# Kernel optimization log

Hardware: AMD Instinct MI355X
Metric: run time of the kernel (lower is better)

The kernel has to match this reference:

```python
import jax, jax.numpy as jnp
import numpy as np

B, S, D_MODEL, N_HEADS, D_FF = 4, 2048, 1024, 16, 4096
HEAD_DIM = D_MODEL // N_HEADS
NUM_BUCKETS, MAX_DISTANCE = 32, 128
EPS = 1e-6


def _relative_position_bucket(relative_position, num_buckets=NUM_BUCKETS, max_distance=MAX_DISTANCE):
    # bidirectional (encoder) variant, matching T5RelativePositionBias
    n = -relative_position
    nb = num_buckets // 2
    ret = (n < 0).astype(jnp.int32) * nb
    n = jnp.abs(n)
    max_exact = nb // 2
    val_if_large = max_exact + (
        jnp.log(jnp.maximum(n, 1).astype(jnp.float32) / max_exact)
        / np.log(max_distance / max_exact) * (nb - max_exact)
    ).astype(jnp.int32)
    val_if_large = jnp.minimum(val_if_large, nb - 1)
    return ret + jnp.where(n < max_exact, n, val_if_large)


def t5_position_bias(rel_emb, q_len, k_len):
    ctx = jnp.arange(q_len)[:, None]
    mem = jnp.arange(k_len)[None, :]
    rp_bucket = _relative_position_bucket(mem - ctx)          # [S, S]
    bias = rel_emb[rp_bucket]                                  # [S, S, H]
    return jnp.transpose(bias, (2, 0, 1))[None]                # [1, H, S, S]


def layer_norm(x, g, b):
    mu = jnp.mean(x, axis=-1, keepdims=True)
    var = jnp.mean(jnp.square(x - mu), axis=-1, keepdims=True)
    return (x - mu) * jax.lax.rsqrt(var + EPS) * g + b


def setup_inputs() -> dict:
    key = jax.random.key(0)
    ks = jax.random.split(key, 20)
    s = 0.02
    p = {
        'src': jax.random.normal(ks[0], (B, S, D_MODEL), jnp.float32),
        'wq': jax.random.normal(ks[1], (D_MODEL, D_MODEL), jnp.float32) * s,
        'bq': jnp.zeros((D_MODEL,), jnp.float32),
        'wk': jax.random.normal(ks[2], (D_MODEL, D_MODEL), jnp.float32) * s,
        'bk': jnp.zeros((D_MODEL,), jnp.float32),
        'wv': jax.random.normal(ks[3], (D_MODEL, D_MODEL), jnp.float32) * s,
        'bv': jnp.zeros((D_MODEL,), jnp.float32),
        'wo': jax.random.normal(ks[4], (D_MODEL, D_MODEL), jnp.float32) * s,
        'bo': jnp.zeros((D_MODEL,), jnp.float32),
        'w1': jax.random.normal(ks[5], (D_MODEL, D_FF), jnp.float32) * s,
        'b1': jnp.zeros((D_FF,), jnp.float32),
        'w2': jax.random.normal(ks[6], (D_FF, D_MODEL), jnp.float32) * s,
        'b2': jnp.zeros((D_MODEL,), jnp.float32),
        'ln1_g': jnp.ones((D_MODEL,), jnp.float32),
        'ln1_b': jnp.zeros((D_MODEL,), jnp.float32),
        'ln2_g': jnp.ones((D_MODEL,), jnp.float32),
        'ln2_b': jnp.zeros((D_MODEL,), jnp.float32),
        'rel_emb': jax.random.normal(ks[7], (NUM_BUCKETS, N_HEADS), jnp.float32) * s,
    }
    return p


def reference(src, wq, bq, wk, bk, wv, bv, wo, bo, w1, b1, w2, b2,
              ln1_g, ln1_b, ln2_g, ln2_b, rel_emb):
    b, s, _ = src.shape

    # --- self-attention block (pre-norm) ---
    xn = layer_norm(src, ln1_g, ln1_b)
    q = (xn @ wq + bq).reshape(b, s, N_HEADS, HEAD_DIM).transpose(0, 2, 1, 3)
    k = (xn @ wk + bk).reshape(b, s, N_HEADS, HEAD_DIM).transpose(0, 2, 1, 3)
    v = (xn @ wv + bv).reshape(b, s, N_HEADS, HEAD_DIM).transpose(0, 2, 1, 3)

    bias = t5_position_bias(rel_emb, s, s)                       # [1,H,S,S]
    scores = jnp.einsum('bhqd,bhkd->bhqk', q, k) / np.sqrt(HEAD_DIM) + bias
    attn = jax.nn.softmax(scores, axis=-1)
    ctx = jnp.einsum('bhqk,bhkd->bhqd', attn, v)                 # [B,H,S,Dh]
    ctx = ctx.transpose(0, 2, 1, 3).reshape(b, s, D_MODEL)
    x = src + (ctx @ wo + bo)

    # --- FFN block (pre-norm, ReLU) ---
    yn = layer_norm(x, ln2_g, ln2_b)
    y = jax.nn.relu(yn @ w1 + b1) @ w2 + b2
    return x + y
```

## Files before the change

### kernel.cpp

```cpp
#include <hip/hip_runtime.h>
#include <math.h>

typedef unsigned short u16;

#define S_LEN 2048
#define BSZ 4
#define DM 1024
#define NH 16
#define HD 64
#define DFF 4096
#define ROWS (BSZ * S_LEN)
#define LOG2E 1.4426950408889634f

typedef __attribute__((__ext_vector_type__(8))) __bf16 bf16x8;
typedef __attribute__((__ext_vector_type__(8))) short short8;
typedef __attribute__((__ext_vector_type__(4))) short short4v;
typedef __attribute__((__ext_vector_type__(4))) float f32x4;
typedef __attribute__((__ext_vector_type__(4))) float float4v;

__device__ __forceinline__ float bf2f(u16 u) {
    union { unsigned int i; float f; } c; c.i = ((unsigned int)u) << 16; return c.f;
}
__device__ __forceinline__ u16 f2bf(float f) {
    union { float f; unsigned int i; } c; c.f = f;
    unsigned int r = c.i + 0x7fffu + ((c.i >> 16) & 1u);
    return (u16)(r >> 16);
}
__device__ __forceinline__ u16 f2bf_rn(float f) {
    union { float f; unsigned int i; } c; c.f = f;
    return (u16)((c.i + 0x8000u) >> 16);
}
__device__ __forceinline__ float ldin(const void* p, long i, int f32) {
    return f32 ? ((const float*)p)[i] : bf2f(((const u16*)p)[i]);
}
__device__ __forceinline__ int dtype_f32(const u16* ln1g) {
    return ln1g[0] != 0x3F80;
}
__device__ __forceinline__ void gl_lds16(const void* g, void* l) {
    __builtin_amdgcn_global_load_lds(
        (const __attribute__((address_space(1))) unsigned int*)g,
        (__attribute__((address_space(3))) unsigned int*)l, 16, 0, 0);
}

#define DPP_ADD(x, ctrl) { int _v = __builtin_bit_cast(int, x);                         \
    float _y = __builtin_bit_cast(float, __builtin_amdgcn_mov_dpp(_v, ctrl, 0xF, 0xF, true)); \
    x = x + _y; }

__device__ __forceinline__ void tr_tile(
    const void* __restrict__ src, u16* __restrict__ dst, int N, int K,
    int bx, int by, int f32, int tid, u16 (*t)[72])
{
#pragma unroll
    for (int i = 0; i < 2; i++) {
        int c = tid + i * 256;
        int row = c >> 3, col = (c & 7) * 8;
        long off = (long)(by * 64 + row) * N + bx * 64 + col;
        short8 v;
        if (f32) {
            const float* s = (const float*)src + off;
            float4v a = *(const float4v*)s;
            float4v b = *(const float4v*)(s + 4);
#pragma unroll
            for (int k = 0; k < 4; k++) { v[k] = (short)f2bf(a[k]); v[k + 4] = (short)f2bf(b[k]); }
        } else {
            v = *(const short8*)((const u16*)src + off);
        }
        *(short8*)(&t[row][col]) = v;
    }
    __syncthreads();
#pragma unroll
    for (int i = 0; i < 2; i++) {
        int c = tid + i * 256;
        int row = c >> 3, col = (c & 7) * 8;
        short8 v;
#pragma unroll
        for (int jj = 0; jj < 8; jj++) v[jj] = (short)t[col + jj][row];
        *(short8*)(dst + (long)(bx * 64 + row) * K + by * 64 + col) = v;
    }
}

__global__ __launch_bounds__(256) void transpose4(
    const void* wq, const void* wk, const void* wv, const void* wo,
    u16* __restrict__ wqkvt, u16* __restrict__ wot, const u16* __restrict__ ln1g)
{
    __shared__ u16 t[64][72];
    int z = blockIdx.z;
    const void* src = (z == 0) ? wq : (z == 1) ? wk : (z == 2) ? wv : wo;
    u16* dst = (z < 3) ? wqkvt + (long)z * 1024 * 1024 : wot;
    tr_tile(src, dst, DM, DM, blockIdx.x, blockIdx.y, dtype_f32(ln1g), threadIdx.x, t);
}

__global__ __launch_bounds__(256) void transpose2(
    const void* w1, const void* w2, u16* __restrict__ w1t, u16* __restrict__ w2t,
    const u16* __restrict__ ln1g)
{
    __shared__ u16 t[64][72];
    int f32 = dtype_f32(ln1g);
    if (blockIdx.z == 0)
        tr_tile(w1, w1t, DFF, DM, blockIdx.x, blockIdx.y, f32, threadIdx.x, t);
    else
        tr_tile(w2, w2t, DM, DFF, blockIdx.y, blockIdx.x, f32, threadIdx.x, t);
}

__global__ __launch_bounds__(256) void vtrans(
    const u16* __restrict__ v, u16* __restrict__ vt)
{
    __shared__ u16 t[64][72];
    int s0 = blockIdx.x * 64;
    int bh = blockIdx.y;
    const u16* src = v + (long)bh * S_LEN * HD;
    u16* dst = vt + (long)bh * HD * S_LEN;
    int tid = threadIdx.x;
#pragma unroll
    for (int i = 0; i < 2; i++) {
        int c = tid + i * 256;
        int row = c >> 3, col = (c & 7) * 8;
        *(short8*)(&t[row][col]) = *(const short8*)(src + (long)(s0 + row) * HD + col);
    }
    __syncthreads();
#pragma unroll
    for (int i = 0; i < 2; i++) {
        int c = tid + i * 256;
        int row = c >> 3, col = (c & 7) * 8;
        short8 o;
#pragma unroll
        for (int jj = 0; jj < 8; jj++) o[jj] = (short)t[col + jj][row];
        *(short8*)(dst + (long)row * S_LEN + s0 + col) = o;
    }
}

__global__ __launch_bounds__(256) void prep_kernel(
    const void* bq, const void* bk, const void* bv, const void* bo,
    const void* b1, const void* b2, const void* l1g, const void* l1b,
    const void* l2g, const void* l2b, const void* rel,
    u16* __restrict__ smalls, float* __restrict__ bias_full)
{
    int f32 = dtype_f32((const u16*)l1g);
    int tid = blockIdx.x * blockDim.x + threadIdx.x;
    if (tid < 13312) {
        float v;
        if      (tid < 1024)  v = ldin(bq,  tid,         f32);
        else if (tid < 2048)  v = ldin(bk,  tid - 1024,  f32);
        else if (tid < 3072)  v = ldin(bv,  tid - 2048,  f32);
        else if (tid < 4096)  v = ldin(bo,  tid - 3072,  f32);
        else if (tid < 8192)  v = ldin(b1,  tid - 4096,  f32);
        else if (tid < 9216)  v = ldin(b2,  tid - 8192,  f32);
        else if (tid < 10240) v = ldin(l1g, tid - 9216,  f32);
        else if (tid < 11264) v = ldin(l1b, tid - 10240, f32);
        else if (tid < 12288) v = ldin(l2g, tid - 11264, f32);
        else                  v = ldin(l2b, tid - 12288, f32);
        smalls[tid] = f2bf(v);
    }
    if (tid < 4095 * 16) {
        int dIdx = tid >> 4;
        int h = tid & 15;
        int delta = dIdx - 2047;
        int n = -delta;
        int ret = (n < 0) ? 16 : 0;
        int na = (n < 0) ? -n : n;
        int bkt;
        if (na < 8) {
            bkt = na;
        } else {
            float tval = logf((float)na * 0.125f) * 2.8853900817779268f;
            int v = 8 + (int)tval;
            bkt = v < 15 ? v : 15;
        }
        bkt += ret;
        bias_full[h * 4095 + dIdx] = ldin(rel, bkt * 16 + h, f32) * LOG2E;
    }
}

__global__ __launch_bounds__(256) void ln_kernel(
    const void* __restrict__ xin, int external, const u16* __restrict__ ln1g,
    const u16* __restrict__ g, const u16* __restrict__ bta, u16* __restrict__ out)
{
    int f32 = external ? dtype_f32(ln1g) : 0;
    int row = blockIdx.x;
    int tid = threadIdx.x;
    float vals[4];
    if (f32) {
        float4v v = *(const float4v*)((const float*)xin + (long)row * DM + tid * 4);
#pragma unroll
        for (int k = 0; k < 4; k++) vals[k] = v[k];
    } else {
        short4v v = *(const short4v*)((const u16*)xin + (long)row * DM + tid * 4);
#pragma unroll
        for (int k = 0; k < 4; k++) vals[k] = bf2f((u16)v[k]);
    }
    float s1 = 0.f, s2 = 0.f;
#pragma unroll
    for (int k = 0; k < 4; k++) { s1 += vals[k]; s2 += vals[k] * vals[k]; }
#pragma unroll
    for (int off = 32; off > 0; off >>= 1) {
        s1 += __shfl_xor(s1, off);
        s2 += __shfl_xor(s2, off);
    }
    __shared__ float ps1[4], ps2[4];
    int wave = tid >> 6, lane = tid & 63;
    if (lane == 0) { ps1[wave] = s1; ps2[wave] = s2; }
    __syncthreads();
    s1 = ps1[0] + ps1[1] + ps1[2] + ps1[3];
    s2 = ps2[0] + ps2[1] + ps2[2] + ps2[3];
    float mu = s1 * (1.0f / DM);
    float var = s2 * (1.0f / DM) - mu * mu;
    float rs = rsqrtf(var + 1e-6f);
    short4v ov;
#pragma unroll
    for (int k = 0; k < 4; k++) {
        float gv = bf2f(g[tid * 4 + k]);
        float bv = bf2f(bta[tid * 4 + k]);
        ov[k] = (short)f2bf((vals[k] - mu) * rs * gv + bv);
    }
    *(short4v*)(out + (long)row * DM + tid * 4) = ov;
}

#define BM 128
#define BN 128
#define BK 64

__global__ __launch_bounds__(256, 3) void gemm_bt(
    const u16* __restrict__ A, const u16* __restrict__ Bt,
    const u16* __restrict__ bias, int M, int N, int K, int mode,
    u16* __restrict__ out_q, u16* __restrict__ out_k, u16* __restrict__ out_v,
    const void* __restrict__ res, void* __restrict__ outp,
    const u16* __restrict__ ln1g)
{
    __shared__ u16 As[BM][BK];
    __shared__ u16 Bs[BN][BK];
    int tid = threadIdx.x;
    int wave = tid >> 6, lane = tid & 63;
    int quad = lane >> 4, l16 = lane & 15;
    int wr = (wave >> 1) * 64, wc = (wave & 1) * 64;
    long m0 = (long)blockIdx.y * BM, n0 = (long)blockIdx.x * BN;
    int flg = (mode == 2 || mode == 4) ? dtype_f32(ln1g) : 0;

    int prow = tid >> 3;
    int pchk = tid & 7;
    int cchk = pchk ^ (prow & 7);
    int skc = cchk * 8;
    int pkc = pchk * 8;
    int rxor = l16 & 7;

    f32x4 acc[4][4];
    f32x4 z = {0.f, 0.f, 0.f, 0.f};
#pragma unroll
    for (int i = 0; i < 4; i++)
#pragma unroll
        for (int j = 0; j < 4; j++) acc[i][j] = z;

    for (int k0 = 0; k0 < K; k0 += BK) {
        __syncthreads();
#pragma unroll
        for (int ro = 0; ro < 4; ro++) {
            gl_lds16(A  + (m0 + ro * 32 + prow) * K + k0 + skc, &As[ro * 32 + prow][pkc]);
            gl_lds16(Bt + (n0 + ro * 32 + prow) * K + k0 + skc, &Bs[ro * 32 + prow][pkc]);
        }
        __syncthreads();
#pragma unroll
        for (int t = 0; t < 2; t++) {
            int rc = ((t * 4 + quad) ^ rxor) * 8;
            bf16x8 af[4], bfr[4];
#pragma unroll
            for (int i = 0; i < 4; i++)
                af[i] = __builtin_bit_cast(bf16x8, *(const short8*)(&As[wr + i * 16 + l16][rc]));
#pragma unroll
            for (int j = 0; j < 4; j++)
                bfr[j] = __builtin_bit_cast(bf16x8, *(const short8*)(&Bs[wc + j * 16 + l16][rc]));
#pragma unroll
            for (int i = 0; i < 4; i++)
#pragma unroll
                for (int j = 0; j < 4; j++)
                    acc[i][j] = __builtin_amdgcn_mfma_f32_16x16x32_bf16(af[i], bfr[j], acc[i][j], 0, 0, 0);
        }
    }

#pragma unroll
    for (int i = 0; i < 4; i++) {
#pragma unroll
        for (int j = 0; j < 4; j++) {
#pragma unroll
            for (int r = 0; r < 4; r++) {
                long gr = m0 + wr + i * 16 + quad * 4 + r;
                long gc = n0 + wc + j * 16 + l16;
                float val = acc[i][j][r] + bf2f(bias[gc]);
                if (mode == 1) {
                    int sel = (int)(gc >> 10);
                    int cc = (int)(gc & 1023);
                    int h = cc >> 6, d = cc & 63;
                    int b = (int)(gr >> 11), s = (int)(gr & 2047);
                    u16* dst = (sel == 0) ? out_q : (sel == 1 ? out_k : out_v);
                    dst[(((long)(b * NH + h)) * S_LEN + s) * HD + d] = f2bf(val);
                } else if (mode == 2) {
                    long idx = gr * N + gc;
                    float rv = flg ? ((const float*)res)[idx]
                                   : bf2f(((const u16*)res)[idx]);
                    ((u16*)outp)[idx] = f2bf(val + rv);
                } else if (mode == 3) {
                    ((u16*)outp)[gr * N + gc] = f2bf(val > 0.f ? val : 0.f);
                } else {
                    long idx = gr * N + gc;
                    float o = val + bf2f(((const u16*)res)[idx]);
                    if (flg) ((float*)outp)[idx] = o;
                    else     ((u16*)outp)[idx]  = f2bf(o);
                }
            }
        }
    }
}

__global__ __launch_bounds__(256, 4) void attn_kernel(
    const u16* __restrict__ Qg, const u16* __restrict__ Kg, const u16* __restrict__ Vtg,
    const float* __restrict__ bias_full, u16* __restrict__ ctx)
{
    __shared__ u16 Ks[64][64];
    __shared__ u16 Vt[64][64];
    __shared__ u16 Ps[64][72];
    __shared__ float bias_l[2112];
    __shared__ float l_sh[64];

    int bh = blockIdx.y;
    int b = bh >> 4, h = bh & 15;
    int q0 = blockIdx.x * 64;
    const u16* Q  = Qg  + (long)bh * S_LEN * HD;
    const u16* Kp = Kg  + (long)bh * S_LEN * HD;
    const u16* Vp = Vtg + (long)bh * HD * S_LEN;

    int tid = threadIdx.x;
    int wave = tid >> 6, lane = tid & 63;
    int quad = lane >> 4, l16 = lane & 15;

    for (int i = tid; i < 2112; i += 256)
        bias_l[i] = bias_full[h * 4095 + 1984 + i - q0];
    float Bneg = bias_full[h * 4095 + 0];
    float Bpos = bias_full[h * 4095 + 4094];

    int prow = tid >> 3, pchk = tid & 7;
    int cchk = pchk ^ (prow & 7);
    int rxor = l16 & 7;
    int rc0 = (quad ^ rxor) * 8;
    int rc1 = ((4 + quad) ^ rxor) * 8;

    bf16x8 aq[2];
#pragma unroll
    for (int t = 0; t < 2; t++)
        aq[t] = __builtin_bit_cast(bf16x8,
            *(const short8*)(Q + (long)(q0 + wave * 16 + l16) * HD + t * 32 + quad * 8));

    f32x4 o[4];
    f32x4 z = {0.f, 0.f, 0.f, 0.f};
#pragma unroll
    for (int j = 0; j < 4; j++) o[j] = z;
    float l_acc = 0.f;

    int ib = 63 + quad * 4 - wave * 16 - l16;
    const float c0 = 0.125f * LOG2E;

    for (int t0 = 0; t0 < S_LEN; t0 += 64) {
        __syncthreads();
#pragma unroll
        for (int ro = 0; ro < 2; ro++) {
            gl_lds16(Kp + (long)(t0 + ro * 32 + prow) * HD + cchk * 8,
                     &Ks[ro * 32 + prow][pchk * 8]);
            gl_lds16(Vp + (long)(ro * 32 + prow) * S_LEN + t0 + cchk * 8,
                     &Vt[ro * 32 + prow][pchk * 8]);
        }
        __syncthreads();

        f32x4 s_[4];
#pragma unroll
        for (int j = 0; j < 4; j++) {
            f32x4 a = z;
            bf16x8 kf0 = __builtin_bit_cast(bf16x8, *(const short8*)(&Ks[j * 16 + l16][rc0]));
            a = __builtin_amdgcn_mfma_f32_16x16x32_bf16(kf0, aq[0], a, 0, 0, 0);
            bf16x8 kf1 = __builtin_bit_cast(bf16x8, *(const short8*)(&Ks[j * 16 + l16][rc1]));
            a = __builtin_amdgcn_mfma_f32_16x16x32_bf16(kf1, aq[1], a, 0, 0, 0);
            s_[j] = a;
        }
        int d0 = t0 - q0;
        int nearb = (d0 >= -153 && d0 <= 153);
        float bconst = (d0 > 0) ? Bpos : Bneg;
#pragma unroll
        for (int j = 0; j < 4; j++) {
            short4v pk;
#pragma unroll
            for (int r = 0; r < 4; r++) {
                float bl = nearb ? bias_l[ib + t0 + j * 16 + r] : bconst;
                float p = exp2f(fminf(fmaf(s_[j][r], c0, bl), 100.0f));
                l_acc += p;
                pk[r] = (short)f2bf_rn(p);
            }
            *(short4v*)(&Ps[wave * 16 + l16][j * 16 + quad * 4]) = pk;
        }

        bf16x8 ap[2];
#pragma unroll
        for (int tt = 0; tt < 2; tt++)
            ap[tt] = __builtin_bit_cast(bf16x8,
                *(const short8*)(&Ps[wave * 16 + l16][tt * 32 + quad * 8]));
#pragma unroll
        for (int j = 0; j < 4; j++) {
            f32x4 t = o[j];
            bf16x8 bv0 = __builtin_bit_cast(bf16x8, *(const short8*)(&Vt[j * 16 + l16][rc0]));
            t = __builtin_amdgcn_mfma_f32_16x16x32_bf16(ap[0], bv0, t, 0, 0, 0);
            bf16x8 bv1 = __builtin_bit_cast(bf16x8, *(const short8*)(&Vt[j * 16 + l16][rc1]));
            t = __builtin_amdgcn_mfma_f32_16x16x32_bf16(ap[1], bv1, t, 0, 0, 0);
            o[j] = t;
        }
    }

    l_acc += __shfl_xor(l_acc, 16);
    l_acc += __shfl_xor(l_acc, 32);
    l_sh[wave * 16 + l16] = l_acc;
#pragma unroll
    for (int r = 0; r < 4; r++) {
        int qr = wave * 16 + quad * 4 + r;
        float linv = 1.0f / l_sh[qr];
        long srow = (long)(b * S_LEN + q0 + qr);
#pragma unroll
        for (int j = 0; j < 4; j++)
            ctx[srow * DM + h * HD + j * 16 + l16] = f2bf(o[j][r] * linv);
    }
}

extern "C" void kernel_launch(void* const* d_in, const int* in_sizes, int n_in,
                              void* d_out, int out_size, void* d_ws, size_t ws_size,
                              hipStream_t stream)
{
    const void* src  = d_in[0];
    const void* wq   = d_in[1];
    const void* bq   = d_in[2];
    const void* wk   = d_in[3];
    const void* bk   = d_in[4];
    const void* wv   = d_in[5];
    const void* bv   = d_in[6];
    const void* wo   = d_in[7];
    const void* bo   = d_in[8];
    const void* w1   = d_in[9];
    const void* b1   = d_in[10];
    const void* w2   = d_in[11];
    const void* b2   = d_in[12];
    const void* ln1g = d_in[13];
    const void* ln1b = d_in[14];
    const void* ln2g = d_in[15];
    const void* ln2b = d_in[16];
    const void* rel  = d_in[17];
    const u16* l1g16 = (const u16*)ln1g;

    char* ws = (char*)d_ws;
    const long MB = 1L << 20;
    u16*   smalls = (u16*)  (ws);
    float* bfull  = (float*)(ws + 65536);
    u16*   xn     = (u16*)  (ws + 1  * MB);
    u16*   vtg    = (u16*)  (ws + 1  * MB);
    u16*   qws    = (u16*)  (ws + 17 * MB);
    u16*   kws    = (u16*)  (ws + 33 * MB);
    u16*   vws    = (u16*)  (ws + 49 * MB);
    u16*   hbuf   = (u16*)  (ws + 1  * MB);
    u16*   ctx    = (u16*)  (ws + 65 * MB);
    u16*   yn     = (u16*)  (ws + 65 * MB);
    u16*   xbf    = (u16*)  (ws + 81 * MB);
    u16*   wqkvt  = (u16*)  (ws + 97 * MB);
    u16*   wot    = (u16*)  (ws + 103 * MB);
    u16*   w1t    = (u16*)  (ws + 97 * MB);
    u16*   w2t    = (u16*)  (ws + 105 * MB);

    transpose4<<<dim3(16, 16, 4), 256, 0, stream>>>(wq, wk, wv, wo, wqkvt, wot, l1g16);
    prep_kernel<<<256, 256, 0, stream>>>(bq, bk, bv, bo, b1, b2,
                                         ln1g, ln1b, ln2g, ln2b, rel,
                                         smalls, bfull);

    ln_kernel<<<ROWS, 256, 0, stream>>>(src, 1, l1g16,
                                        smalls + 9216, smalls + 10240, xn);

    gemm_bt<<<dim3(3072 / BN, ROWS / BM), 256, 0, stream>>>(
        xn, wqkvt, smalls + 0, ROWS, 3072, DM, 1,
        qws, kws, vws, nullptr, nullptr, l1g16);

    vtrans<<<dim3(S_LEN / 64, BSZ * NH), 256, 0, stream>>>(vws, vtg);

    attn_kernel<<<dim3(S_LEN / 64, BSZ * NH), 256, 0, stream>>>(qws, kws, vtg, bfull, ctx);

    gemm_bt<<<dim3(DM / BN, ROWS / BM), 256, 0, stream>>>(
        ctx, wot, smalls + 3072, ROWS, DM, DM, 2,
        nullptr, nullptr, nullptr, src, xbf, l1g16);

    transpose2<<<dim3(64, 16, 2), 256, 0, stream>>>(w1, w2, w1t, w2t, l1g16);

    ln_kernel<<<ROWS, 256, 0, stream>>>(xbf, 0, l1g16,
                                        smalls + 11264, smalls + 12288, yn);

    gemm_bt<<<dim3(DFF / BN, ROWS / BM), 256, 0, stream>>>(
        yn, w1t, smalls + 4096, ROWS, DFF, DM, 3,
        nullptr, nullptr, nullptr, nullptr, hbuf, l1g16);

    gemm_bt<<<dim3(DM / BN, ROWS / BM), 256, 0, stream>>>(
        hbuf, w2t, smalls + 8192, ROWS, DM, DFF, 4,
        nullptr, nullptr, nullptr, xbf, d_out, l1g16);
}
```

Baseline: 628.5 us.

## Compute softmax row sums via MFMA, store bias as bf16, swizzle GEMM blocks

The attention kernel now computes the softmax denominator with an extra MFMA against a ones vector, removing the scalar accumulation and the cross-lane shuffle/LDS reduction. It also uses the hardware exp2 intrinsic and a native bf16 conversion, and stores the position bias in LDS as bf16 to shrink the shared-memory footprint. Separately, the GEMM remaps block IDs in an XCD-style swizzle to improve L2 locality. The changes trade a little bias precision and two extra MFMAs per tile for fewer VALU ops and less LDS.

Measured after the change: 597.4 us. 1.05x faster.

```diff
diff --git a/kernel.cpp b/kernel.cpp
--- a/kernel.cpp
+++ b/kernel.cpp
@@ -26,9 +26,9 @@
     unsigned int r = c.i + 0x7fffu + ((c.i >> 16) & 1u);
     return (u16)(r >> 16);
 }
-__device__ __forceinline__ u16 f2bf_rn(float f) {
-    union { float f; unsigned int i; } c; c.f = f;
-    return (u16)((c.i + 0x8000u) >> 16);
+__device__ __forceinline__ u16 f2bf_cvt(float f) {
+    __bf16 h = (__bf16)f;
+    return __builtin_bit_cast(u16, h);
 }
 __device__ __forceinline__ float ldin(const void* p, long i, int f32) {
     return f32 ? ((const float*)p)[i] : bf2f(((const u16*)p)[i]);
@@ -41,10 +41,6 @@
         (const __attribute__((address_space(1))) unsigned int*)g,
         (__attribute__((address_space(3))) unsigned int*)l, 16, 0, 0);
 }
-
-#define DPP_ADD(x, ctrl) { int _v = __builtin_bit_cast(int, x);                         \
-    float _y = __builtin_bit_cast(float, __builtin_amdgcn_mov_dpp(_v, ctrl, 0xF, 0xF, true)); \
-    x = x + _y; }
 
 __device__ __forceinline__ void tr_tile(
     const void* __restrict__ src, u16* __restrict__ dst, int N, int K,
@@ -232,7 +228,14 @@
     int wave = tid >> 6, lane = tid & 63;
     int quad = lane >> 4, l16 = lane & 15;
     int wr = (wave >> 1) * 64, wc = (wave & 1) * 64;
-    long m0 = (long)blockIdx.y * BM, n0 = (long)blockIdx.x * BN;
+
+    int nwg = gridDim.x * gridDim.y;
+    int bid = blockIdx.y * gridDim.x + blockIdx.x;
+    int chunk = nwg >> 3;
+    int swz = (bid & 7) * chunk + (bid >> 3);
+    int bx = swz % gridDim.x, by = swz / gridDim.x;
+
+    long m0 = (long)by * BM, n0 = (long)bx * BN;
     int flg = (mode == 2 || mode == 4) ? dtype_f32(ln1g) : 0;
 
     int prow = tid >> 3;
@@ -316,8 +319,7 @@
     __shared__ u16 Ks[64][64];
     __shared__ u16 Vt[64][64];
     __shared__ u16 Ps[64][72];
-    __shared__ float bias_l[2112];
-    __shared__ float l_sh[64];
+    __shared__ u16 bias_s[2112];
 
     int bh = blockIdx.y;
     int b = bh >> 4, h = bh & 15;
@@ -331,7 +333,7 @@
     int quad = lane >> 4, l16 = lane & 15;
 
     for (int i = tid; i < 2112; i += 256)
-        bias_l[i] = bias_full[h * 4095 + 1984 + i - q0];
+        bias_s[i] = f2bf(bias_full[h * 4095 + 1984 + i - q0]);
     float Bneg = bias_full[h * 4095 + 0];
     float Bpos = bias_full[h * 4095 + 4094];
 
@@ -347,11 +349,15 @@
         aq[t] = __builtin_bit_cast(bf16x8,
             *(const short8*)(Q + (long)(q0 + wave * 16 + l16) * HD + t * 32 + quad * 8));
 
+    bf16x8 ones;
+#pragma unroll
+    for (int i = 0; i < 8; i++) ones[i] = (__bf16)1.0f;
+
     f32x4 o[4];
     f32x4 z = {0.f, 0.f, 0.f, 0.f};
 #pragma unroll
     for (int j = 0; j < 4; j++) o[j] = z;
-    float l_acc = 0.f;
+    f32x4 lacc = z;
 
     int ib = 63 + quad * 4 - wave * 16 - l16;
     const float c0 = 0.125f * LOG2E;
@@ -385,10 +391,9 @@
             short4v pk;
 #pragma unroll
             for (int r = 0; r < 4; r++) {
-                float bl = nearb ? bias_l[ib + t0 + j * 16 + r] : bconst;
-                float p = exp2f(fminf(fmaf(s_[j][r], c0, bl), 100.0f));
-                l_acc += p;
-                pk[r] = (short)f2bf_rn(p);
+                float bl = nearb ? bf2f(bias_s[ib + t0 + j * 16 + r]) : bconst;
+                float p = __builtin_amdgcn_exp2f(fminf(fmaf(s_[j][r], c0, bl), 100.0f));
+                pk[r] = (short)f2bf_cvt(p);
             }
             *(short4v*)(&Ps[wave * 16 + l16][j * 16 + quad * 4]) = pk;
         }
@@ -398,6 +403,8 @@
         for (int tt = 0; tt < 2; tt++)
             ap[tt] = __builtin_bit_cast(bf16x8,
                 *(const short8*)(&Ps[wave * 16 + l16][tt * 32 + quad * 8]));
+        lacc = __builtin_amdgcn_mfma_f32_16x16x32_bf16(ap[0], ones, lacc, 0, 0, 0);
+        lacc = __builtin_amdgcn_mfma_f32_16x16x32_bf16(ap[1], ones, lacc, 0, 0, 0);
 #pragma unroll
         for (int j = 0; j < 4; j++) {
             f32x4 t = o[j];
@@ -409,13 +416,10 @@
         }
     }
 
-    l_acc += __shfl_xor(l_acc, 16);
-    l_acc += __shfl_xor(l_acc, 32);
-    l_sh[wave * 16 + l16] = l_acc;
 #pragma unroll
     for (int r = 0; r < 4; r++) {
         int qr = wave * 16 + quad * 4 + r;
-        float linv = 1.0f / l_sh[qr];
+        float linv = 1.0f / lacc[r];
         long srow = (long)(b * S_LEN + q0 + qr);
 #pragma unroll
         for (int j = 0; j < 4; j++)
```
